# Kernel optimization log

Hardware: AMD Instinct MI355X
Metric: run time of the kernel (lower is better)

The kernel has to match this reference:

```python
import jax, jax.numpy as jnp
import numpy as np

B, S, D = 2, 2048, 1024
H, DH = 16, 64  # n_heads, d_head = d_model // n_heads


def setup_inputs() -> dict:
    key = jax.random.key(0)
    ks = jax.random.split(key, 8)
    sc = lambda d: 1.0 / np.sqrt(d)
    return {
        "x": jax.random.normal(ks[0], (B, S, D), jnp.float32),
        "context": jax.random.normal(ks[1], (B, D), jnp.float32),
        "prev_state": jax.random.normal(ks[2], (B, S, D), jnp.float32),
        "attention_mask": jnp.ones((B, 1, S, S), dtype=bool),
        "Wq": jax.random.normal(ks[3], (D, D), jnp.float32) * sc(D),
        "Wk": jax.random.normal(ks[4], (D, D), jnp.float32) * sc(D),
        "Wv": jax.random.normal(ks[5], (D, D), jnp.float32) * sc(D),
        "Wo": jax.random.normal(ks[6], (D, D), jnp.float32) * sc(D),
        "Wc": jax.random.normal(ks[7], (D, DH), jnp.float32) * sc(D),
        "alpha": jnp.ones((1,), jnp.float32),
        "beta": jnp.ones((1,), jnp.float32),
    }


def reference(x, context, prev_state, attention_mask, Wq, Wk, Wv, Wo, Wc, alpha, beta):
    b, s, d = x.shape
    # projections (Linear with no bias, weight stored as [out, in] -> x @ W.T)
    q = (x @ Wq.T).reshape(b, s, H, DH).transpose(0, 2, 1, 3)  # (B,H,S,DH)
    k = (x @ Wk.T).reshape(b, s, H, DH).transpose(0, 2, 1, 3)
    v = (x @ Wv.T).reshape(b, s, H, DH).transpose(0, 2, 1, 3)

    inv_sqrt_dh = 1.0 / jnp.sqrt(jnp.asarray(DH, x.dtype))
    scores = jnp.einsum("bhqd,bhkd->bhqk", q, k) * inv_sqrt_dh

    # CFM: context-flow matching bias, rank-1 per-pair term from global context
    c = context @ Wc  # (B, DH)
    qc = jnp.einsum("bhqd,bd->bhq", q, c)
    kc = jnp.einsum("bhkd,bd->bhk", k, c)
    cfm = qc[..., :, None] * kc[..., None, :] / DH  # (B,H,S,S)

    # AFM: anti-flow matching bias from previous layer state (first d_head dims)
    p = prev_state[..., :DH]  # (B,S,DH)
    afm = jnp.einsum("bhqd,bkd->bhqk", q, p) * inv_sqrt_dh

    scores = scores + alpha[0] * cfm - beta[0] * afm
    scores = jnp.where(attention_mask, scores, jnp.asarray(-1e9, scores.dtype))

    w = jax.nn.softmax(scores, axis=-1)
    out = jnp.einsum("bhqk,bhkd->bhqd", w, v)  # (B,H,S,DH)
    out = out.transpose(0, 2, 1, 3).reshape(b, s, d)
    return out @ Wo.T
```

## Files before the change

### kernel.cpp

```cpp
#include <hip/hip_runtime.h>
#include <stdint.h>

#define D_  1024
#define S_  2048
#define B_  2
#define H_  16
#define DH_ 64
#define M_  (B_*S_)

typedef __bf16 bf16x8 __attribute__((ext_vector_type(8)));
typedef float  f32x4  __attribute__((ext_vector_type(4)));
typedef float  f32x16 __attribute__((ext_vector_type(16)));
typedef short  short8 __attribute__((ext_vector_type(8)));
typedef unsigned uint4v __attribute__((ext_vector_type(4)));
typedef unsigned short u16;

static __device__ __forceinline__ u16 f2bf(float f){
  union { float f; unsigned u; } v; v.f = f;
  unsigned r = v.u + 0x7FFF + ((v.u >> 16) & 1);
  return (u16)(r >> 16);
}
static __device__ __forceinline__ f32x4 mfma16(short8 a, short8 b, f32x4 c){
  return __builtin_amdgcn_mfma_f32_16x16x32_bf16(
      __builtin_bit_cast(bf16x8, a), __builtin_bit_cast(bf16x8, b), c, 0, 0, 0);
}
static __device__ __forceinline__ f32x16 mfma32(short8 a, short8 b, f32x16 c){
  return __builtin_amdgcn_mfma_f32_32x32x16_bf16(
      __builtin_bit_cast(bf16x8, a), __builtin_bit_cast(bf16x8, b), c, 0, 0, 0);
}
static __device__ __forceinline__ f32x16 zero16(){
  f32x16 z = {0,0,0,0,0,0,0,0,0,0,0,0,0,0,0,0};
  return z;
}
static __device__ __forceinline__ float fexp2(float x){
#if __has_builtin(__builtin_amdgcn_exp2f)
  return __builtin_amdgcn_exp2f(x);
#else
  return __exp2f(x);
#endif
}
static __device__ __forceinline__ unsigned cvtpk(float lo, float hi){
  unsigned r;
  asm("v_cvt_pk_bf16_f32 %0, %1, %2" : "=v"(r) : "v"(lo), "v"(hi));
  return r;
}
static __device__ __forceinline__ void gl_lds16(const u16* g, u16* lds){
  __builtin_amdgcn_global_load_lds(
      (const __attribute__((address_space(1))) void*)(uintptr_t)g,
      (__attribute__((address_space(3))) void*)(uintptr_t)lds, 16, 0, 0);
}

__global__ void k_f2bf(const float* __restrict__ in, u16* __restrict__ out, int n4){
  int i = blockIdx.x * blockDim.x + threadIdx.x;
  if(i >= n4) return;
  float4 v = ((const float4*)in)[i];
  ushort4 o; o.x = f2bf(v.x); o.y = f2bf(v.y); o.z = f2bf(v.z); o.w = f2bf(v.w);
  ((ushort4*)out)[i] = o;
}

__global__ void k_f2bf4(const float* __restrict__ a0, const float* __restrict__ a1,
                        const float* __restrict__ a2, const float* __restrict__ a3,
                        u16* __restrict__ o0, u16* __restrict__ o1,
                        u16* __restrict__ o2, u16* __restrict__ o3, int n4){
  const float* in; u16* out;
  switch(blockIdx.y){
    case 0: in=a0; out=o0; break;
    case 1: in=a1; out=o1; break;
    case 2: in=a2; out=o2; break;
    default: in=a3; out=o3; break;
  }
  int i = blockIdx.x * blockDim.x + threadIdx.x;
  if(i >= n4) return;
  float4 v = ((const float4*)in)[i];
  ushort4 o; o.x = f2bf(v.x); o.y = f2bf(v.y); o.z = f2bf(v.z); o.w = f2bf(v.w);
  ((ushort4*)out)[i] = o;
}

__global__ void k_ctx(const float* __restrict__ context, const float* __restrict__ Wc,
                      float* __restrict__ cvec, int* __restrict__ flags){
  __shared__ float partial[4][2][64];
  int t = threadIdx.x;
  if(t < 2) flags[t] = 1;
  int c = t >> 7;
  int b = (t >> 6) & 1;
  int j = t & 63;
  float s = 0.f;
  #pragma unroll 8
  for(int d = c*256; d < (c+1)*256; ++d) s += context[b*D_ + d] * Wc[d*DH_ + j];
  partial[c][b][j] = s;
  __syncthreads();
  if(t < 128){
    int b2 = t >> 6, j2 = t & 63;
    cvec[b2*DH_ + j2] = partial[0][b2][j2] + partial[1][b2][j2]
                      + partial[2][b2][j2] + partial[3][b2][j2];
  }
}

__global__ void k_mask_check(const uint4* __restrict__ m, int n16, int* flags){
  int i = blockIdx.x * blockDim.x + threadIdx.x;
  bool ok8 = true, ok32 = true;
  if(i < n16){
    uint4 v = m[i];
    ok8  = (v.x==0x01010101u)&&(v.y==0x01010101u)&&(v.z==0x01010101u)&&(v.w==0x01010101u);
    ok32 = (v.x==1u)&&(v.y==1u)&&(v.z==1u)&&(v.w==1u);
  }
  unsigned long long b8  = __ballot(!ok8);
  unsigned long long b32 = __ballot(!ok32);
  if((threadIdx.x & 63) == 0){
    if(b8)  flags[0] = 0;
    if(b32) flags[1] = 0;
  }
}

__global__ __launch_bounds__(256,3) void k_gemm_qkv(const u16* __restrict__ A,
    const u16* __restrict__ Wcat, u16* __restrict__ Qb, u16* __restrict__ Kb,
    u16* __restrict__ VT, const float* __restrict__ cvec,
    const float* __restrict__ prev, const float* __restrict__ beta_p,
    float* __restrict__ qcb, float* __restrict__ kcb){
  __shared__ u16 As[128*64];
  __shared__ u16 Bs[128*64];
  __shared__ float red[2][2][64];
  const int tid = threadIdx.x;
  const int w = tid >> 6, l = tid & 63;
  const int wr = w >> 1, wc = w & 1;
  const int id = blockIdx.x;
  const int bn = id >> 5;
  const int bm = id & 31;
  const int lr = l & 15, lh = l >> 4;
  const int srow = l >> 3, scol = (l & 7) * 8;

  f32x4 acc[4][4] = {};

  for(int kt = 0; kt < 16; ++kt){
    const int k0 = kt * 64;
    #pragma unroll
    for(int i = 0; i < 4; ++i){
      const int chunk = i*4 + w;
      gl_lds16(A    + (size_t)(bm*128 + chunk*8 + srow)*D_ + k0 + scol, &As[chunk*512]);
      gl_lds16(Wcat + (size_t)(bn*128 + chunk*8 + srow)*D_ + k0 + scol, &Bs[chunk*512]);
    }
    __syncthreads();
    #pragma unroll
    for(int kk = 0; kk < 2; ++kk){
      short8 a[4], b[4];
      #pragma unroll
      for(int m = 0; m < 4; ++m)
        a[m] = *(const short8*)&As[(wr*64 + m*16 + lr)*64 + kk*32 + lh*8];
      #pragma unroll
      for(int n = 0; n < 4; ++n)
        b[n] = *(const short8*)&Bs[(wc*64 + n*16 + lr)*64 + kk*32 + lh*8];
      #pragma unroll
      for(int m = 0; m < 4; ++m)
        #pragma unroll
        for(int n = 0; n < 4; ++n)
          acc[m][n] = mfma16(a[m], b[n], acc[m][n]);
    }
    __syncthreads();
  }

  const int b = bm >> 4;

  if(bn < 16){
    float cv[4];
    #pragma unroll
    for(int n = 0; n < 4; ++n) cv[n] = cvec[b*DH_ + n*16 + lr];
    float part[4][4];
    #pragma unroll
    for(int m = 0; m < 4; ++m)
      #pragma unroll
      for(int r = 0; r < 4; ++r){
        float p = acc[m][0][r]*cv[0] + acc[m][1][r]*cv[1]
                + acc[m][2][r]*cv[2] + acc[m][3][r]*cv[3];
        p += __shfl_xor(p, 1, 64); p += __shfl_xor(p, 2, 64);
        p += __shfl_xor(p, 4, 64); p += __shfl_xor(p, 8, 64);
        part[m][r] = p;
      }
    if(lr == 0){
      #pragma unroll
      for(int m = 0; m < 4; ++m)
        #pragma unroll
        for(int r = 0; r < 4; ++r)
          red[wr][wc][m*16 + lh*4 + r] = part[m][r];
    }
    __syncthreads();
    {
      int wr2 = tid >> 7, wc2 = (tid >> 6) & 1, i = tid & 63;
      int s = (bm & 15)*128 + wr2*64 + i;
      int head = (bn & 7)*2 + wc2;
      float* qkc = (bn < 8) ? qcb : kcb;
      qkc[((size_t)b*H_ + head)*S_ + s] = red[wr2][wc2][i];
    }
  }

  if(bn < 8){
    #pragma unroll
    for(int m = 0; m < 4; ++m){
      const size_t row0 = (size_t)bm*128 + wr*64 + m*16 + lh*4;
      #pragma unroll
      for(int n = 0; n < 4; ++n){
        const size_t col = (size_t)bn*128 + wc*64 + n*16 + lr;
        #pragma unroll
        for(int r = 0; r < 4; ++r)
          Qb[(row0 + r)*D_ + col] = f2bf(acc[m][n][r]);
      }
    }
  } else if(bn < 16){
    const float beta = beta_p[0];
    const float KSCALE = 0.125f * 1.44269504088896340736f;
    #pragma unroll
    for(int m = 0; m < 4; ++m){
      const size_t row0 = (size_t)bm*128 + wr*64 + m*16 + lh*4;
      #pragma unroll
      for(int n = 0; n < 4; ++n){
        const size_t col = (size_t)(bn - 8)*128 + wc*64 + n*16 + lr;
        #pragma unroll
        for(int r = 0; r < 4; ++r){
          float v = (acc[m][n][r] - beta * prev[(row0 + r)*D_ + n*16 + lr]) * KSCALE;
          Kb[(row0 + r)*D_ + col] = f2bf(v);
        }
      }
    }
  } else {
    #pragma unroll
    for(int m = 0; m < 4; ++m){
      const int s0 = (bm & 15)*128 + wr*64 + m*16 + lh*4;
      #pragma unroll
      for(int n = 0; n < 4; ++n){
        const int col = (bn - 16)*128 + wc*64 + n*16 + lr;
        ushort4 o;
        o.x = f2bf(acc[m][n][0]); o.y = f2bf(acc[m][n][1]);
        o.z = f2bf(acc[m][n][2]); o.w = f2bf(acc[m][n][3]);
        *(ushort4*)&VT[((size_t)(b*1024 + col))*S_ + s0] = o;
      }
    }
  }
}

__global__ __launch_bounds__(256,2) void k_gemm_o(const u16* __restrict__ A,
    const u16* __restrict__ W, float* __restrict__ Cout){
  __shared__ u16 As[128*64];
  __shared__ u16 Bs[64*64];
  const int tid = threadIdx.x;
  const int w = tid >> 6, l = tid & 63;
  const int wr = w >> 1, wc = w & 1;
  const int bm = blockIdx.x >> 4;
  const int bn = blockIdx.x & 15;
  const int lr = l & 15, lh = l >> 4;
  const int srow = l >> 3, scol = (l & 7) * 8;

  f32x4 acc[4][2] = {};

  for(int kt = 0; kt < 16; ++kt){
    const int k0 = kt * 64;
    #pragma unroll
    for(int i = 0; i < 4; ++i){
      const int chunk = i*4 + w;
      gl_lds16(A + (size_t)(bm*128 + chunk*8 + srow)*D_ + k0 + scol, &As[chunk*512]);
    }
    #pragma unroll
    for(int i = 0; i < 2; ++i){
      const int chunk = w*2 + i;
      gl_lds16(W + (size_t)(bn*64 + chunk*8 + srow)*D_ + k0 + scol, &Bs[chunk*512]);
    }
    __syncthreads();
    #pragma unroll
    for(int kk = 0; kk < 2; ++kk){
      short8 a[4], b[2];
      #pragma unroll
      for(int m = 0; m < 4; ++m)
        a[m] = *(const short8*)&As[(wr*64 + m*16 + lr)*64 + kk*32 + lh*8];
      #pragma unroll
      for(int n = 0; n < 2; ++n)
        b[n] = *(const short8*)&Bs[(wc*32 + n*16 + lr)*64 + kk*32 + lh*8];
      #pragma unroll
      for(int m = 0; m < 4; ++m)
        #pragma unroll
        for(int n = 0; n < 2; ++n)
          acc[m][n] = mfma16(a[m], b[n], acc[m][n]);
    }
    __syncthreads();
  }
  #pragma unroll
  for(int m = 0; m < 4; ++m){
    const size_t row0 = (size_t)bm*128 + wr*64 + m*16 + lh*4;
    #pragma unroll
    for(int n = 0; n < 2; ++n){
      const size_t col = (size_t)bn*64 + wc*32 + n*16 + lr;
      #pragma unroll
      for(int r = 0; r < 4; ++r)
        Cout[(row0 + r)*D_ + col] = acc[m][n][r];
    }
  }
}

template<bool AM>
__device__ __forceinline__ void attn_pipe(
    const u16* __restrict__ Kb_h, const u16* __restrict__ VT_h,
    const float* __restrict__ kcp, const unsigned char* __restrict__ maskr,
    u16* __restrict__ KB, u16* __restrict__ VB,
    const short8 (&qa)[4], float aq, f32x16 (&oacc)[2], float& lp,
    int q32, int hi, int hb, int srow, int sdh, int wv, int xk){
  #define STG(T, BUF) { _Pragma("unroll") for(int j = 0; j < 4; ++j){            \
      const int ck = j*2 + wv;                                                   \
      gl_lds16(Kb_h + (size_t)((T)*64 + ck*8 + srow)*D_ + sdh,                   \
               KB + (BUF)*4096 + ck*512);                                        \
      gl_lds16(VT_h + (size_t)(ck*8 + srow)*S_ + (T)*64 + sdh,                   \
               VB + (BUF)*4096 + ck*512); } }
  STG(0, 0);
  STG(1, 1);
  asm volatile("s_waitcnt vmcnt(8)" ::: "memory");
  __builtin_amdgcn_s_barrier();

  for(int kt = 0; kt < 32; ++kt){
    const int buf = kt % 3;
    const int k0 = kt*64;
    if(kt < 30) STG(kt+2, (kt+2) % 3);

    f32x16 sacc[2] = {zero16(), zero16()};
    #pragma unroll
    for(int kg = 0; kg < 2; ++kg)
      #pragma unroll
      for(int c = 0; c < 4; ++c){
        short8 kf = *(const short8*)&KB[buf*4096 + (kg*32 + q32)*64 + ((c*16 + hb) ^ xk)];
        sacc[kg] = mfma32(kf, qa[c], sacc[kg]);
      }
    short8 vf[2][4];
    #pragma unroll
    for(int dh2 = 0; dh2 < 2; ++dh2)
      #pragma unroll
      for(int c = 0; c < 4; ++c)
        vf[dh2][c] = *(const short8*)&VB[buf*4096 + (dh2*32 + q32)*64 + ((c*16 + hb) ^ xk)];

    unsigned pk[2][8];
    #pragma unroll
    for(int kg = 0; kg < 2; ++kg){
      float p[16];
      #pragma unroll
      for(int rg = 0; rg < 4; ++rg){
        f32x4 kv = *(const f32x4*)&kcp[k0 + kg*32 + rg*8 + hi*4];
        unsigned mu = 0x01010101u;
        if(AM) mu = *(const unsigned*)&maskr[k0 + kg*32 + rg*8 + hi*4];
        #pragma unroll
        for(int j = 0; j < 4; ++j){
          float tv = sacc[kg][rg*4 + j] + aq*kv[j];
          if(AM){ if(((mu >> (8*j)) & 255u) == 0u) tv = -160.0f; }
          float e = fexp2(tv);
          lp += e;
          p[rg*4 + j] = e;
        }
      }
      #pragma unroll
      for(int i = 0; i < 8; ++i) pk[kg][i] = cvtpk(p[2*i], p[2*i+1]);
    }

    #pragma unroll
    for(int c = 0; c < 4; ++c){
      const int kg = c >> 1, c4 = (c & 1)*4;
      unsigned x0 = pk[kg][c4+0], y0 = pk[kg][c4+2];
      unsigned x1 = pk[kg][c4+1], y1 = pk[kg][c4+3];
      asm("v_permlane32_swap_b32 %0, %1" : "+v"(x0), "+v"(y0));
      asm("v_permlane32_swap_b32 %0, %1" : "+v"(x1), "+v"(y1));
      uint4v pb = {x0, x1, y0, y1};
      short8 pbf = __builtin_bit_cast(short8, pb);
      #pragma unroll
      for(int dh2 = 0; dh2 < 2; ++dh2)
        oacc[dh2] = mfma32(vf[dh2][c], pbf, oacc[dh2]);
    }

    if(kt < 30) asm volatile("s_waitcnt vmcnt(8)" ::: "memory");
    else        asm volatile("s_waitcnt vmcnt(0)" ::: "memory");
    __builtin_amdgcn_s_barrier();
  }
  #undef STG
}

__global__ __launch_bounds__(128,2) void k_attn(const u16* __restrict__ Qb,
    const u16* __restrict__ Kb, const u16* __restrict__ VT,
    const float* __restrict__ qc, const float* __restrict__ kc,
    const float* __restrict__ alpha_p, const unsigned char* __restrict__ mask,
    const int* __restrict__ flags, u16* __restrict__ Ob){
  __shared__ u16 Kbuf[3][4096];
  __shared__ u16 Vbuf[3][4096];
  const int tid = threadIdx.x;
  const int wv = tid >> 6, l = tid & 63;
  const int q32 = l & 31, hi = l >> 5, hb = hi*8;
  const int id = blockIdx.x;
  const int bh = id & 31, qb = id >> 5;
  const int b = bh >> 4, h = bh & 15;
  const int q0w = qb*64 + wv*32;
  const float aL = alpha_p[0] * (1.0f/64.0f) * 1.44269504088896340736f;
  const bool allones = (flags[0] | flags[1]) != 0;
  const u16* Kb_h = Kb + (size_t)b*S_*D_ + h*DH_;
  const u16* VT_h = VT + ((size_t)(b*1024 + h*DH_))*S_;
  const float* kcp = kc + (size_t)bh*S_;
  const unsigned char* maskr = mask + ((size_t)b*S_ + q0w + q32)*S_;

  const int srow = l >> 3;
  const int sdh  = ((l & 7) ^ srow) * 8;
  const int xk   = (q32 & 7) << 3;

  short8 qa[4];
  #pragma unroll
  for(int c = 0; c < 4; ++c)
    qa[c] = *(const short8*)&Qb[((size_t)b*S_ + q0w + q32)*D_ + h*DH_ + c*16 + hb];
  const float aq = aL * qc[(size_t)bh*S_ + q0w + q32];

  f32x16 oacc[2] = {zero16(), zero16()};
  float lp = 0.f;

  if(allones)
    attn_pipe<false>(Kb_h, VT_h, kcp, maskr, &Kbuf[0][0], &Vbuf[0][0],
                     qa, aq, oacc, lp, q32, hi, hb, srow, sdh, wv, xk);
  else
    attn_pipe<true>(Kb_h, VT_h, kcp, maskr, &Kbuf[0][0], &Vbuf[0][0],
                    qa, aq, oacc, lp, q32, hi, hb, srow, sdh, wv, xk);

  float lt = lp + __shfl_xor(lp, 32, 64);
  float inv = 1.0f / lt;
  u16* orow = Ob + ((size_t)b*S_ + q0w + q32)*D_ + h*DH_;
  #pragma unroll
  for(int dh2 = 0; dh2 < 2; ++dh2)
    #pragma unroll
    for(int rg = 0; rg < 4; ++rg){
      ushort4 o;
      o.x = f2bf(oacc[dh2][rg*4+0]*inv);
      o.y = f2bf(oacc[dh2][rg*4+1]*inv);
      o.z = f2bf(oacc[dh2][rg*4+2]*inv);
      o.w = f2bf(oacc[dh2][rg*4+3]*inv);
      *(ushort4*)&orow[dh2*32 + rg*8 + hi*4] = o;
    }
}

extern "C" void kernel_launch(void* const* d_in, const int* in_sizes, int n_in,
                              void* d_out, int out_size, void* d_ws, size_t ws_size,
                              hipStream_t stream){
  const float* x    = (const float*)d_in[0];
  const float* ctx  = (const float*)d_in[1];
  const float* prev = (const float*)d_in[2];
  const unsigned char* mask = (const unsigned char*)d_in[3];
  const float* Wq = (const float*)d_in[4];
  const float* Wk = (const float*)d_in[5];
  const float* Wv = (const float*)d_in[6];
  const float* Wo = (const float*)d_in[7];
  const float* Wc = (const float*)d_in[8];
  const float* alpha = (const float*)d_in[9];
  const float* beta  = (const float*)d_in[10];

  char* ws = (char*)d_ws;
  size_t off = 0;
  auto alloc = [&](size_t bytes)->void*{
    void* p = ws + off; off += (bytes + 255) & ~(size_t)255; return p;
  };
  u16* xb   = (u16*)alloc((size_t)M_*D_*2);
  u16* wcat = (u16*)alloc((size_t)3*D_*D_*2);
  u16* wob  = (u16*)alloc((size_t)D_*D_*2);
  u16* Qb   = (u16*)alloc((size_t)M_*D_*2);
  u16* Kb   = (u16*)alloc((size_t)M_*D_*2);
  u16* VT   = (u16*)alloc((size_t)B_*D_*S_*2);
  float* qcb  = (float*)alloc((size_t)B_*H_*S_*4);
  float* kcb  = (float*)alloc((size_t)B_*H_*S_*4);
  float* cvec = (float*)alloc(512);
  int*  flags = (int*)alloc(64);
  u16* Ob = xb;

  k_f2bf<<<M_*D_/4/256, 256, 0, stream>>>(x, xb, M_*D_/4);
  {
    dim3 g(D_*D_/4/256, 4);
    k_f2bf4<<<g, 256, 0, stream>>>(Wq, Wk, Wv, Wo,
        wcat, wcat + (size_t)D_*D_, wcat + (size_t)2*D_*D_, wob, D_*D_/4);
  }
  k_ctx<<<1, 512, 0, stream>>>(ctx, Wc, cvec, flags);
  {
    int n16 = B_*S_*S_/16;
    k_mask_check<<<n16/256, 256, 0, stream>>>((const uint4*)mask, n16, flags);
  }
  k_gemm_qkv<<<768, 256, 0, stream>>>(xb, wcat, Qb, Kb, VT, cvec, prev, beta, qcb, kcb);
  k_attn<<<1024, 128, 0, stream>>>(Qb, Kb, VT, qcb, kcb, alpha, mask, flags, Ob);
  k_gemm_o<<<512, 256, 0, stream>>>(Ob, wob, (float*)d_out);
}
```

Baseline: 157.9 us.

## Restructure attention to single-wave blocks with direct-register V loads

```diff
diff --git a/kernel.cpp b/kernel.cpp
--- a/kernel.cpp
+++ b/kernel.cpp
@@ -294,106 +294,97 @@
 }
 
 template<bool AM>
-__device__ __forceinline__ void attn_pipe(
+__device__ __forceinline__ void attn_1w(
     const u16* __restrict__ Kb_h, const u16* __restrict__ VT_h,
     const float* __restrict__ kcp, const unsigned char* __restrict__ maskr,
-    u16* __restrict__ KB, u16* __restrict__ VB,
-    const short8 (&qa)[4], float aq, f32x16 (&oacc)[2], float& lp,
-    int q32, int hi, int hb, int srow, int sdh, int wv, int xk){
-  #define STG(T, BUF) { _Pragma("unroll") for(int j = 0; j < 4; ++j){            \
-      const int ck = j*2 + wv;                                                   \
-      gl_lds16(Kb_h + (size_t)((T)*64 + ck*8 + srow)*D_ + sdh,                   \
-               KB + (BUF)*4096 + ck*512);                                        \
-      gl_lds16(VT_h + (size_t)(ck*8 + srow)*S_ + (T)*64 + sdh,                   \
-               VB + (BUF)*4096 + ck*512); } }
-  STG(0, 0);
-  STG(1, 1);
-  asm volatile("s_waitcnt vmcnt(8)" ::: "memory");
-  __builtin_amdgcn_s_barrier();
-
-  for(int kt = 0; kt < 32; ++kt){
-    const int buf = kt % 3;
-    const int k0 = kt*64;
-    if(kt < 30) STG(kt+2, (kt+2) % 3);
-
-    f32x16 sacc[2] = {zero16(), zero16()};
-    #pragma unroll
-    for(int kg = 0; kg < 2; ++kg)
-      #pragma unroll
-      for(int c = 0; c < 4; ++c){
-        short8 kf = *(const short8*)&KB[buf*4096 + (kg*32 + q32)*64 + ((c*16 + hb) ^ xk)];
-        sacc[kg] = mfma32(kf, qa[c], sacc[kg]);
-      }
-    short8 vf[2][4];
-    #pragma unroll
-    for(int dh2 = 0; dh2 < 2; ++dh2)
-      #pragma unroll
-      for(int c = 0; c < 4; ++c)
-        vf[dh2][c] = *(const short8*)&VB[buf*4096 + (dh2*32 + q32)*64 + ((c*16 + hb) ^ xk)];
-
-    unsigned pk[2][8];
-    #pragma unroll
-    for(int kg = 0; kg < 2; ++kg){
-      float p[16];
-      #pragma unroll
-      for(int rg = 0; rg < 4; ++rg){
-        f32x4 kv = *(const f32x4*)&kcp[k0 + kg*32 + rg*8 + hi*4];
-        unsigned mu = 0x01010101u;
-        if(AM) mu = *(const unsigned*)&maskr[k0 + kg*32 + rg*8 + hi*4];
-        #pragma unroll
-        for(int j = 0; j < 4; ++j){
-          float tv = sacc[kg][rg*4 + j] + aq*kv[j];
-          if(AM){ if(((mu >> (8*j)) & 255u) == 0u) tv = -160.0f; }
-          float e = fexp2(tv);
-          lp += e;
-          p[rg*4 + j] = e;
-        }
-      }
-      #pragma unroll
-      for(int i = 0; i < 8; ++i) pk[kg][i] = cvtpk(p[2*i], p[2*i+1]);
-    }
-
-    #pragma unroll
-    for(int c = 0; c < 4; ++c){
-      const int kg = c >> 1, c4 = (c & 1)*4;
-      unsigned x0 = pk[kg][c4+0], y0 = pk[kg][c4+2];
-      unsigned x1 = pk[kg][c4+1], y1 = pk[kg][c4+3];
-      asm("v_permlane32_swap_b32 %0, %1" : "+v"(x0), "+v"(y0));
-      asm("v_permlane32_swap_b32 %0, %1" : "+v"(x1), "+v"(y1));
-      uint4v pb = {x0, x1, y0, y1};
-      short8 pbf = __builtin_bit_cast(short8, pb);
-      #pragma unroll
-      for(int dh2 = 0; dh2 < 2; ++dh2)
-        oacc[dh2] = mfma32(vf[dh2][c], pbf, oacc[dh2]);
-    }
-
-    if(kt < 30) asm volatile("s_waitcnt vmcnt(8)" ::: "memory");
-    else        asm volatile("s_waitcnt vmcnt(0)" ::: "memory");
-    __builtin_amdgcn_s_barrier();
-  }
-  #undef STG
-}
-
-__global__ __launch_bounds__(128,2) void k_attn(const u16* __restrict__ Qb,
+    u16* __restrict__ KB, const short8 (&qa)[4], float aq,
+    f32x16 (&oacc)[2], float& lp,
+    int q32, int hi, int hb, int srow, int sdh, int xk){
+  short8 vfA[2][4], vfB[2][4];
+
+  #define STGK(T, BUF) { _Pragma("unroll") for(int j = 0; j < 8; ++j)            \
+      gl_lds16(Kb_h + (size_t)((T)*64 + j*8 + srow)*D_ + sdh,                    \
+               KB + (BUF)*4096 + j*512); }
+  #define LOADV(T, VF) { _Pragma("unroll") for(int d2 = 0; d2 < 2; ++d2){        \
+      _Pragma("unroll") for(int c = 0; c < 4; ++c)                               \
+        VF[d2][c] = *(const short8*)&VT_h[(size_t)(d2*32 + q32)*S_               \
+                                          + (size_t)(T)*64 + c*16 + hb]; } }
+
+  STGK(0, 0);
+  LOADV(0, vfA);
+
+  #define BODY(T, BUF, VCUR, VNXT) {                                             \
+    if((T) < 31){                                                                \
+      STGK((T)+1, (BUF)^1);                                                      \
+      LOADV((T)+1, VNXT);                                                        \
+      asm volatile("s_waitcnt vmcnt(16)" ::: "memory");                          \
+    } else {                                                                     \
+      asm volatile("s_waitcnt vmcnt(0)" ::: "memory");                           \
+    }                                                                            \
+    const int k0 = (T)*64;                                                       \
+    unsigned pk[2][8];                                                           \
+    _Pragma("unroll") for(int kg = 0; kg < 2; ++kg){                             \
+      f32x16 sacc = zero16();                                                    \
+      _Pragma("unroll") for(int c = 0; c < 4; ++c){                              \
+        short8 kf = *(const short8*)&KB[(BUF)*4096 + (kg*32 + q32)*64            \
+                                        + ((c*16 + hb) ^ xk)];                   \
+        sacc = mfma32(kf, qa[c], sacc);                                          \
+      }                                                                          \
+      float p[16];                                                               \
+      _Pragma("unroll") for(int rg = 0; rg < 4; ++rg){                           \
+        f32x4 kv = *(const f32x4*)&kcp[k0 + kg*32 + rg*8 + hi*4];                \
+        unsigned mu = 0x01010101u;                                               \
+        if(AM) mu = *(const unsigned*)&maskr[k0 + kg*32 + rg*8 + hi*4];          \
+        _Pragma("unroll") for(int j = 0; j < 4; ++j){                            \
+          float tv = sacc[rg*4 + j] + aq*kv[j];                                  \
+          if(AM){ if(((mu >> (8*j)) & 255u) == 0u) tv = -160.0f; }               \
+          float e = fexp2(tv);                                                   \
+          lp += e; p[rg*4 + j] = e;                                              \
+        }                                                                        \
+      }                                                                          \
+      _Pragma("unroll") for(int i = 0; i < 8; ++i)                               \
+        pk[kg][i] = cvtpk(p[2*i], p[2*i+1]);                                     \
+    }                                                                            \
+    _Pragma("unroll") for(int c = 0; c < 4; ++c){                                \
+      const int kg = c >> 1, c4 = (c & 1)*4;                                     \
+      unsigned x0 = pk[kg][c4+0], y0 = pk[kg][c4+2];                             \
+      unsigned x1 = pk[kg][c4+1], y1 = pk[kg][c4+3];                             \
+      asm("v_permlane32_swap_b32 %0, %1" : "+v"(x0), "+v"(y0));                  \
+      asm("v_permlane32_swap_b32 %0, %1" : "+v"(x1), "+v"(y1));                  \
+      uint4v pb = {x0, x1, y0, y1};                                              \
+      short8 pbf = __builtin_bit_cast(short8, pb);                               \
+      _Pragma("unroll") for(int d2 = 0; d2 < 2; ++d2)                            \
+        oacc[d2] = mfma32(VCUR[d2][c], pbf, oacc[d2]);                           \
+    }                                                                            \
+  }
+
+  for(int t2 = 0; t2 < 16; ++t2){
+    BODY(2*t2,   0, vfA, vfB);
+    BODY(2*t2+1, 1, vfB, vfA);
+  }
+  #undef BODY
+  #undef LOADV
+  #undef STGK
+}
+
+__global__ __launch_bounds__(64,2) void k_attn(const u16* __restrict__ Qb,
     const u16* __restrict__ Kb, const u16* __restrict__ VT,
     const float* __restrict__ qc, const float* __restrict__ kc,
     const float* __restrict__ alpha_p, const unsigned char* __restrict__ mask,
     const int* __restrict__ flags, u16* __restrict__ Ob){
-  __shared__ u16 Kbuf[3][4096];
-  __shared__ u16 Vbuf[3][4096];
-  const int tid = threadIdx.x;
-  const int wv = tid >> 6, l = tid & 63;
+  __shared__ u16 Kbuf[2][4096];
+  const int l = threadIdx.x;
   const int q32 = l & 31, hi = l >> 5, hb = hi*8;
   const int id = blockIdx.x;
   const int bh = id & 31, qb = id >> 5;
   const int b = bh >> 4, h = bh & 15;
-  const int q0w = qb*64 + wv*32;
+  const int q0 = qb*32;
   const float aL = alpha_p[0] * (1.0f/64.0f) * 1.44269504088896340736f;
   const bool allones = (flags[0] | flags[1]) != 0;
   const u16* Kb_h = Kb + (size_t)b*S_*D_ + h*DH_;
   const u16* VT_h = VT + ((size_t)(b*1024 + h*DH_))*S_;
   const float* kcp = kc + (size_t)bh*S_;
-  const unsigned char* maskr = mask + ((size_t)b*S_ + q0w + q32)*S_;
+  const unsigned char* maskr = mask + ((size_t)b*S_ + q0 + q32)*S_;
 
   const int srow = l >> 3;
   const int sdh  = ((l & 7) ^ srow) * 8;
@@ -402,22 +393,22 @@
   short8 qa[4];
   #pragma unroll
   for(int c = 0; c < 4; ++c)
-    qa[c] = *(const short8*)&Qb[((size_t)b*S_ + q0w + q32)*D_ + h*DH_ + c*16 + hb];
-  const float aq = aL * qc[(size_t)bh*S_ + q0w + q32];
+    qa[c] = *(const short8*)&Qb[((size_t)b*S_ + q0 + q32)*D_ + h*DH_ + c*16 + hb];
+  const float aq = aL * qc[(size_t)bh*S_ + q0 + q32];
 
   f32x16 oacc[2] = {zero16(), zero16()};
   float lp = 0.f;
 
   if(allones)
-    attn_pipe<false>(Kb_h, VT_h, kcp, maskr, &Kbuf[0][0], &Vbuf[0][0],
-                     qa, aq, oacc, lp, q32, hi, hb, srow, sdh, wv, xk);
+    attn_1w<false>(Kb_h, VT_h, kcp, maskr, &Kbuf[0][0], qa, aq, oacc, lp,
+                   q32, hi, hb, srow, sdh, xk);
   else
-    attn_pipe<true>(Kb_h, VT_h, kcp, maskr, &Kbuf[0][0], &Vbuf[0][0],
-                    qa, aq, oacc, lp, q32, hi, hb, srow, sdh, wv, xk);
+    attn_1w<true>(Kb_h, VT_h, kcp, maskr, &Kbuf[0][0], qa, aq, oacc, lp,
+                  q32, hi, hb, srow, sdh, xk);
 
   float lt = lp + __shfl_xor(lp, 32, 64);
   float inv = 1.0f / lt;
-  u16* orow = Ob + ((size_t)b*S_ + q0w + q32)*D_ + h*DH_;
+  u16* orow = Ob + ((size_t)b*S_ + q0 + q32)*D_ + h*DH_;
   #pragma unroll
   for(int dh2 = 0; dh2 < 2; ++dh2)
     #pragma unroll
@@ -475,6 +466,6 @@
     k_mask_check<<<n16/256, 256, 0, stream>>>((const uint4*)mask, n16, flags);
   }
   k_gemm_qkv<<<768, 256, 0, stream>>>(xb, wcat, Qb, Kb, VT, cvec, prev, beta, qcb, kcb);
-  k_attn<<<1024, 128, 0, stream>>>(Qb, Kb, VT, qcb, kcb, alpha, mask, flags, Ob);
+  k_attn<<<2048, 64, 0, stream>>>(Qb, Kb, VT, qcb, kcb, alpha, mask, flags, Ob);
   k_gemm_o<<<512, 256, 0, stream>>>(Ob, wob, (float*)d_out);
 }
```

Measured after the change: 180.6 us. 14.4% more time.
